# Performance work log

Hardware: AMD Instinct MI355X
Metric: run time of the kernel (lower is better)

Reference implementation:

```python
import jax, jax.numpy as jnp
import numpy as np

TOP_K = 4
N_GROUP = 8
TOPK_GROUP = 4
SCALE = 1.0

B, S, H, I, E = 2, 1024, 1024, 512, 32
SHARED_I = I * 2  # n_shared_experts = 2


def setup_inputs() -> dict:
    key = jax.random.key(0)
    ks = jax.random.split(key, 9)
    return {
        "hidden_states": jax.random.normal(ks[0], (B, S, H), jnp.float32),
        "gate_w": jax.random.normal(ks[1], (E, H), jnp.float32) * 0.02,
        "gate_bias": jnp.zeros((E,), jnp.float32),
        "gate_proj": jax.random.normal(ks[2], (E, I, H), jnp.float32) * 0.02,
        "up_proj": jax.random.normal(ks[3], (E, I, H), jnp.float32) * 0.02,
        "down_proj": jax.random.normal(ks[4], (E, H, I), jnp.float32) * 0.02,
        "shared_gate_w": jax.random.normal(ks[5], (SHARED_I, H), jnp.float32) * 0.02,
        "shared_up_w": jax.random.normal(ks[6], (SHARED_I, H), jnp.float32) * 0.02,
        "shared_down_w": jax.random.normal(ks[7], (H, SHARED_I), jnp.float32) * 0.02,
    }


def reference(hidden_states, gate_w, gate_bias, gate_proj, up_proj, down_proj,
              shared_gate_w, shared_up_w, shared_down_w):
    b, s, h = hidden_states.shape
    e = gate_w.shape[0]
    x = hidden_states.reshape(-1, h)            # (T, H)
    t = x.shape[0]

    # ---- gating (DeepSeek-V3 grouped sigmoid routing) ----
    logits = x @ gate_w.T                       # (T, E)
    scores = jax.nn.sigmoid(logits)
    sfc = scores + gate_bias[None, :]           # scores_for_choice
    # per-group score = sum of top-2 experts in group
    group_scores = jax.lax.top_k(sfc.reshape(t, N_GROUP, -1), 2)[0].sum(-1)  # (T, G)
    _, gidx = jax.lax.top_k(group_scores, TOPK_GROUP)                        # (T, topk_group)
    gmask = jax.nn.one_hot(gidx, N_GROUP, dtype=sfc.dtype).sum(1)            # (T, G)
    smask = jnp.repeat(gmask, e // N_GROUP, axis=1)                          # (T, E)
    tmp = jnp.where(smask > 0, sfc, 0.0)
    _, topk_idx = jax.lax.top_k(tmp, TOP_K)                                  # (T, K)
    topk_w = jnp.take_along_axis(scores, topk_idx, axis=1)                   # (T, K)
    topk_w = topk_w / (topk_w.sum(-1, keepdims=True) + 1e-20)                # norm_topk_prob
    topk_w = topk_w * SCALE

    # ---- routed experts (dense combine-weight formulation) ----
    comb = jnp.zeros((t, e), x.dtype).at[jnp.arange(t)[:, None], topk_idx].add(topk_w)  # (T, E)
    g = jnp.einsum('th,eih->eti', x, gate_proj)   # (E, T, I)
    u = jnp.einsum('th,eih->eti', x, up_proj)     # (E, T, I)
    a = jax.nn.silu(g) * u
    a = a * comb.T[:, :, None]                    # scale before down-proj to skip zero experts
    out = jnp.einsum('eti,ehi->th', a, down_proj) # (T, H)

    # ---- shared experts ----
    sg = x @ shared_gate_w.T
    su = x @ shared_up_w.T
    out = out + (jax.nn.silu(sg) * su) @ shared_down_w.T

    return out.reshape(b, s, h)
```

## Files before the change

kernel.cpp:

```cpp
#include <hip/hip_runtime.h>
#include <hip/hip_bf16.h>
#include <cstdint>
#include <cstddef>

#define H_DIM 1024
#define I_DIM 512
#define E_NUM 32
#define SHARED_I_DIM 1024
#define TOPK 4
#define NGROUP 8
#define TOPKG 4
#define GT 8

typedef __attribute__((ext_vector_type(8))) short bf16x8;
typedef __attribute__((ext_vector_type(4))) float f32x4;
typedef __attribute__((ext_vector_type(8))) unsigned short u16x8;

__device__ inline unsigned short f2bf(float f) {
    __hip_bfloat16 h = __float2bfloat16(f);
    return *reinterpret_cast<unsigned short*>(&h);
}
__device__ inline float bf2f(unsigned short u) {
    union { unsigned int u; float f; } w;
    w.u = ((unsigned int)u) << 16;
    return w.f;
}

__device__ inline int laddr(int row, int chunk) {
    return row * 64 + ((chunk ^ (row & 7)) << 3);
}

__global__ void init_kernel(int* cnt) {
    if (threadIdx.x < 64) cnt[threadIdx.x] = 0;
}

__global__ void cvt_kernel(const float* __restrict__ src, unsigned short* __restrict__ dst, int n8) {
    int i = blockIdx.x * blockDim.x + threadIdx.x;
    if (i >= n8) return;
    float4 a = *(const float4*)(src + (size_t)i * 8);
    float4 b = *(const float4*)(src + (size_t)i * 8 + 4);
    u16x8 v;
    v[0] = f2bf(a.x); v[1] = f2bf(a.y); v[2] = f2bf(a.z); v[3] = f2bf(a.w);
    v[4] = f2bf(b.x); v[5] = f2bf(b.y); v[6] = f2bf(b.z); v[7] = f2bf(b.w);
    *(u16x8*)(dst + (size_t)i * 8) = v;
}

__global__ __launch_bounds__(256) void gate_kernel(const float* __restrict__ x,
                                                   const float* __restrict__ gw,
                                                   float* __restrict__ logits_out) {
    int tb = blockIdx.x;
    int tid = threadIdx.x;
    __shared__ float xs[GT][H_DIM];
    __shared__ float ps[8][GT][E_NUM];
    const float* xsrc = x + (size_t)tb * GT * H_DIM;
    for (int i = tid; i < GT * H_DIM / 4; i += 256)
        ((float4*)&xs[0][0])[i] = ((const float4*)xsrc)[i];
    __syncthreads();
    int e = tid & 31, part = tid >> 5;
    const float* wrow = gw + (size_t)e * H_DIM + part * 128;
    float acc[GT] = {};
    for (int c0 = 0; c0 < 128; c0 += 32) {
        float w[32];
#pragma unroll
        for (int c = 0; c < 32; c++) w[c] = wrow[c0 + c];
#pragma unroll
        for (int t = 0; t < GT; t++) {
#pragma unroll
            for (int c = 0; c < 32; c++)
                acc[t] += w[c] * xs[t][part * 128 + c0 + c];
        }
    }
#pragma unroll
    for (int t = 0; t < GT; t++) ps[part][t][e] = acc[t];
    __syncthreads();
    {
        int t = tid >> 5, ee = tid & 31;
        float s = 0.f;
#pragma unroll
        for (int p = 0; p < 8; p++) s += ps[p][t][ee];
        logits_out[((size_t)tb * GT + t) * E_NUM + ee] = s;
    }
}

__global__ void select_kernel(const float* __restrict__ logits, const float* __restrict__ gb,
                              int* __restrict__ topk_e, float* __restrict__ topk_w,
                              int* __restrict__ cnt, int T) {
    int t = blockIdx.x * blockDim.x + threadIdx.x;
    if (t >= T) return;
    float scores[E_NUM], sfc[E_NUM];
#pragma unroll
    for (int i = 0; i < E_NUM; i++) {
        float l = logits[(size_t)t * E_NUM + i];
        float s = 1.f / (1.f + expf(-l));
        scores[i] = s;
        sfc[i] = s + gb[i];
    }
    float gs[NGROUP];
#pragma unroll
    for (int g = 0; g < NGROUP; g++) {
        float m1 = -1e30f, m2 = -1e30f;
#pragma unroll
        for (int j = 0; j < 4; j++) {
            float v = sfc[g * 4 + j];
            if (v > m1) { m2 = m1; m1 = v; }
            else if (v > m2) { m2 = v; }
        }
        gs[g] = m1 + m2;
    }
    unsigned gmask = 0;
    for (int r = 0; r < TOPKG; r++) {
        int best = 0; float bv = -1e30f;
#pragma unroll
        for (int g = 0; g < NGROUP; g++)
            if (!((gmask >> g) & 1u) && gs[g] > bv) { bv = gs[g]; best = g; }
        gmask |= 1u << best;
    }
    unsigned cmask = 0;
    int eidx[TOPK]; float ew[TOPK]; float sum = 0.f;
    for (int r = 0; r < TOPK; r++) {
        int best = 0; float bv = -1e30f; float bsc = 0.f;
#pragma unroll
        for (int i = 0; i < E_NUM; i++) {
            float v = ((gmask >> (i >> 2)) & 1u) ? sfc[i] : 0.0f;
            if (!((cmask >> i) & 1u) && v > bv) { bv = v; best = i; bsc = scores[i]; }
        }
        cmask |= 1u << best;
        eidx[r] = best; ew[r] = bsc; sum += bsc;
    }
    float inv = 1.f / (sum + 1e-20f);
#pragma unroll
    for (int k = 0; k < TOPK; k++) {
        topk_e[t * TOPK + k] = eidx[k];
        topk_w[t * TOPK + k] = ew[k] * inv;
        atomicAdd(&cnt[eidx[k]], 1);
    }
}

__global__ void scan_kernel(const int* __restrict__ cnt, int* __restrict__ off) {
    if (threadIdx.x == 0) {
        int a = 0;
        for (int e = 0; e < E_NUM; e++) { off[e] = a; a += cnt[e]; }
        off[E_NUM] = a;
    }
}

__global__ void bin_kernel(const int* __restrict__ topk_e, const float* __restrict__ topk_w,
                           const int* __restrict__ off, int* __restrict__ cnt2,
                           int* __restrict__ slot_token, float* __restrict__ slot_w,
                           int* __restrict__ slot_of, int total) {
    int i = blockIdx.x * blockDim.x + threadIdx.x;
    if (i >= total) return;
    int e = topk_e[i];
    float w = topk_w[i];
    int pos = atomicAdd(&cnt2[e], 1);
    int slot = off[e] + pos;
    slot_token[slot] = i >> 2;
    slot_w[slot] = w;
    slot_of[i] = slot;
}

__global__ __launch_bounds__(256) void combine_kernel(const unsigned short* __restrict__ out_slot,
                                                      const int* __restrict__ slot_of,
                                                      float* __restrict__ out) {
    int t = blockIdx.x;
    int h = threadIdx.x * 4;
    int s0 = slot_of[t * TOPK + 0], s1 = slot_of[t * TOPK + 1];
    int s2 = slot_of[t * TOPK + 2], s3 = slot_of[t * TOPK + 3];
    ushort4 a = *(const ushort4*)(out_slot + (size_t)s0 * H_DIM + h);
    ushort4 b = *(const ushort4*)(out_slot + (size_t)s1 * H_DIM + h);
    ushort4 c = *(const ushort4*)(out_slot + (size_t)s2 * H_DIM + h);
    ushort4 d = *(const ushort4*)(out_slot + (size_t)s3 * H_DIM + h);
    float4 o = *(float4*)(out + (size_t)t * H_DIM + h);
    o.x += bf2f(a.x) + bf2f(b.x) + bf2f(c.x) + bf2f(d.x);
    o.y += bf2f(a.y) + bf2f(b.y) + bf2f(c.y) + bf2f(d.y);
    o.z += bf2f(a.z) + bf2f(b.z) + bf2f(c.z) + bf2f(d.z);
    o.w += bf2f(a.w) + bf2f(b.w) + bf2f(c.w) + bf2f(d.w);
    *(float4*)(out + (size_t)t * H_DIM + h) = o;
}

template <int MODE, bool DUAL, int BM, bool ROUTED, bool AGATHER>
__global__ __launch_bounds__(512, 2) void gemm_kernel(
    const unsigned short* __restrict__ A, const float* __restrict__ B1,
    const float* __restrict__ B2, size_t bstride,
    void* __restrict__ Dst, int ldD,
    const int* __restrict__ slot_token, const float* __restrict__ slot_w,
    const int* __restrict__ cnt, const int* __restrict__ off_arr, int K, int Mtot) {
    static_assert(MODE != 0 || DUAL, "MODE0 requires DUAL");
    constexpr int RW = BM / 4;
    constexpr int MF = RW / 16;
    constexpr int ACH = BM / 64;
    constexpr int TPR = 512 / BM;

    int itile, mtile, e;
    if constexpr (ROUTED) { e = blockIdx.x; itile = blockIdx.y; mtile = blockIdx.z; }
    else                  { itile = blockIdx.x; mtile = blockIdx.y; e = 0; }
    int count = Mtot, base = 0;
    if (ROUTED) {
        count = cnt[e];
        base = off_arr[e];
        if (mtile * BM >= count) return;
    }

    __shared__ __align__(16) unsigned short As[2][BM * 64];
    __shared__ __align__(16) unsigned short Bs1[2][64 * 64];
    __shared__ __align__(16) unsigned short Bs2[2][DUAL ? 64 * 64 : 8];

    int tid = threadIdx.x;

    int as_row = tid / TPR;
    int as_cb = (tid % TPR) * ACH;
    int am = mtile * BM + as_row;
    int ar;
    if (AGATHER)      ar = (am < count) ? slot_token[base + am] : 0;
    else if (ROUTED)  ar = base + ((am < count) ? am : 0);
    else              ar = (am < count) ? am : 0;
    const unsigned short* Arow = A + (size_t)ar * K + as_cb * 8;

    int bs_row = tid >> 3, bs_ch = tid & 7;
    const float* B1r = B1 + (size_t)e * bstride + (size_t)(itile * 64 + bs_row) * K + bs_ch * 8;
    const float* B2r = DUAL ? (B2 + (size_t)e * bstride + (size_t)(itile * 64 + bs_row) * K + bs_ch * 8)
                            : nullptr;

    f32x4 acc1[MF][2] = {};
    f32x4 acc2[DUAL ? MF : 1][2] = {};

    int lane = tid & 63, wid = tid >> 6;
    int wrow = (wid >> 1) * RW, wcol = (wid & 1) * 32;
    int frow = lane & 15, fch = lane >> 4;

    u16x8 pA0[ACH], pA1[ACH];
    float4 b1lo0, b1hi0, b1lo1, b1hi1;
    float4 b2lo0, b2hi0, b2lo1, b2hi1;

    auto loadS = [&](u16x8* pA, float4& b1lo, float4& b1hi, float4& b2lo, float4& b2hi, int k0) {
#pragma unroll
        for (int c = 0; c < ACH; c++) pA[c] = *(const u16x8*)(Arow + k0 + c * 8);
        b1lo = *(const float4*)(B1r + k0);
        b1hi = *(const float4*)(B1r + k0 + 4);
        if constexpr (DUAL) {
            b2lo = *(const float4*)(B2r + k0);
            b2hi = *(const float4*)(B2r + k0 + 4);
        }
    };
    auto writeS = [&](int buf, const u16x8* pA, float4 b1lo, float4 b1hi, float4 b2lo, float4 b2hi) {
        unsigned short* As_ = As[buf];
        unsigned short* Bs1_ = Bs1[buf];
#pragma unroll
        for (int c = 0; c < ACH; c++)
            *(u16x8*)(&As_[laddr(as_row, as_cb + c)]) = pA[c];
        u16x8 s;
        s[0] = f2bf(b1lo.x); s[1] = f2bf(b1lo.y); s[2] = f2bf(b1lo.z); s[3] = f2bf(b1lo.w);
        s[4] = f2bf(b1hi.x); s[5] = f2bf(b1hi.y); s[6] = f2bf(b1hi.z); s[7] = f2bf(b1hi.w);
        *(u16x8*)(&Bs1_[laddr(bs_row, bs_ch)]) = s;
        if constexpr (DUAL) {
            unsigned short* Bs2_ = Bs2[buf];
            u16x8 s2;
            s2[0] = f2bf(b2lo.x); s2[1] = f2bf(b2lo.y); s2[2] = f2bf(b2lo.z); s2[3] = f2bf(b2lo.w);
            s2[4] = f2bf(b2hi.x); s2[5] = f2bf(b2hi.y); s2[6] = f2bf(b2hi.z); s2[7] = f2bf(b2hi.w);
            *(u16x8*)(&Bs2_[laddr(bs_row, bs_ch)]) = s2;
        }
    };
    auto compute = [&](int buf) {
        const unsigned short* As_ = As[buf];
        const unsigned short* Bs1_ = Bs1[buf];
        const unsigned short* Bs2_ = Bs2[buf];
#pragma unroll
        for (int kk = 0; kk < 2; kk++) {
            int cb = fch + kk * 4;
            bf16x8 bf1[2], bf2[DUAL ? 2 : 1], af[MF];
#pragma unroll
            for (int nf = 0; nf < 2; nf++)
                bf1[nf] = *(const bf16x8*)(&Bs1_[laddr(wcol + nf * 16 + frow, cb)]);
            if constexpr (DUAL) {
#pragma unroll
                for (int nf = 0; nf < 2; nf++)
                    bf2[nf] = *(const bf16x8*)(&Bs2_[laddr(wcol + nf * 16 + frow, cb)]);
            }
#pragma unroll
            for (int mf = 0; mf < MF; mf++)
                af[mf] = *(const bf16x8*)(&As_[laddr(wrow + mf * 16 + frow, cb)]);
#pragma unroll
            for (int mf = 0; mf < MF; mf++)
#pragma unroll
                for (int nf = 0; nf < 2; nf++) {
                    acc1[mf][nf] = __builtin_amdgcn_mfma_f32_16x16x32_bf16(af[mf], bf1[nf], acc1[mf][nf], 0, 0, 0);
                    if constexpr (DUAL)
                        acc2[mf][nf] = __builtin_amdgcn_mfma_f32_16x16x32_bf16(af[mf], bf2[nf], acc2[mf][nf], 0, 0, 0);
                }
        }
    };

    const int NK = K >> 6;
    loadS(pA0, b1lo0, b1hi0, b2lo0, b2hi0, 0);
    loadS(pA1, b1lo1, b1hi1, b2lo1, b2hi1, 64);
    writeS(0, pA0, b1lo0, b1hi0, b2lo0, b2hi0);
    loadS(pA0, b1lo0, b1hi0, b2lo0, b2hi0, 128);
    __syncthreads();
    for (int it = 0; it < NK; it += 2) {
        writeS(1, pA1, b1lo1, b1hi1, b2lo1, b2hi1);
        if (it + 3 < NK) loadS(pA1, b1lo1, b1hi1, b2lo1, b2hi1, (it + 3) << 6);
        compute(0);
        __syncthreads();
        if (it + 2 < NK) {
            writeS(0, pA0, b1lo0, b1hi0, b2lo0, b2hi0);
            if (it + 4 < NK) loadS(pA0, b1lo0, b1hi0, b2lo0, b2hi0, (it + 4) << 6);
        }
        compute(1);
        if (it + 2 < NK) __syncthreads();
    }

#pragma unroll
    for (int mf = 0; mf < MF; mf++)
#pragma unroll
        for (int nf = 0; nf < 2; nf++)
#pragma unroll
            for (int j = 0; j < 4; j++) {
                int rloc = wrow + mf * 16 + (lane >> 4) * 4 + j;
                int mrow = mtile * BM + rloc;
                int col = itile * 64 + wcol + nf * 16 + (lane & 15);
                if (mrow >= count) continue;
                if constexpr (MODE == 0) {
                    float w = ROUTED ? slot_w[base + mrow] : 1.0f;
                    float g = acc1[mf][nf][j];
                    float a = (g / (1.f + __expf(-g))) * acc2[mf][nf][j] * w;
                    ((unsigned short*)Dst)[(size_t)(base + mrow) * ldD + col] = f2bf(a);
                } else if constexpr (MODE == 1) {
                    ((float*)Dst)[(size_t)mrow * ldD + col] = acc1[mf][nf][j];
                } else {
                    ((unsigned short*)Dst)[(size_t)(base + mrow) * ldD + col] = f2bf(acc1[mf][nf][j]);
                }
            }
}

extern "C" void kernel_launch(void* const* d_in, const int* in_sizes, int n_in,
                              void* d_out, int out_size, void* d_ws, size_t ws_size,
                              hipStream_t stream) {
    const float* x = (const float*)d_in[0];
    const float* gw = (const float*)d_in[1];
    const float* gb = (const float*)d_in[2];
    const float* gate_proj = (const float*)d_in[3];
    const float* up_proj = (const float*)d_in[4];
    const float* down_proj = (const float*)d_in[5];
    const float* sgw = (const float*)d_in[6];
    const float* suw = (const float*)d_in[7];
    const float* sdw = (const float*)d_in[8];
    float* out = (float*)d_out;

    const int T = in_sizes[0] / H_DIM;
    const int total_slots = T * TOPK;

    char* ws = (char*)d_ws;
    int* cnt = (int*)ws;
    int* cnt2 = cnt + 32;
    int* off = cnt + 64;
    int* topk_e = cnt + 128;
    float* topk_w = (float*)(topk_e + total_slots);
    int* slot_token = (int*)(topk_w + total_slots);
    float* slot_w = (float*)(slot_token + total_slots);
    int* slot_of = (int*)(slot_w + total_slots);
    float* logits = (float*)(slot_of + total_slots);
    unsigned short* x_bf = (unsigned short*)(logits + (size_t)T * E_NUM);
    unsigned short* act_r = x_bf + (size_t)T * H_DIM;
    unsigned short* act_s = act_r + (size_t)(total_slots + 256) * I_DIM;
    unsigned short* out_slot = act_s + (size_t)T * SHARED_I_DIM;

    hipLaunchKernelGGL(init_kernel, dim3(1), dim3(64), 0, stream, cnt);
    hipLaunchKernelGGL(cvt_kernel, dim3((T * H_DIM / 8 + 255) / 256), dim3(256), 0, stream,
                       x, x_bf, T * H_DIM / 8);
    hipLaunchKernelGGL(gate_kernel, dim3(T / GT), dim3(256), 0, stream, x, gw, logits);
    hipLaunchKernelGGL(select_kernel, dim3((T + 255) / 256), dim3(256), 0, stream,
                       logits, gb, topk_e, topk_w, cnt, T);
    hipLaunchKernelGGL(scan_kernel, dim3(1), dim3(1), 0, stream, cnt, off);
    hipLaunchKernelGGL(bin_kernel, dim3((total_slots + 255) / 256), dim3(256), 0, stream,
                       topk_e, topk_w, off, cnt2, slot_token, slot_w, slot_of, total_slots);

    hipLaunchKernelGGL((gemm_kernel<0, true, 256, true, true>),
                       dim3(E_NUM, I_DIM / 64, 32), dim3(512), 0, stream,
                       x_bf, gate_proj, up_proj, (size_t)I_DIM * H_DIM,
                       (void*)act_r, I_DIM, slot_token, slot_w, cnt, off, H_DIM, 0);

    hipLaunchKernelGGL((gemm_kernel<0, true, 128, false, false>),
                       dim3(SHARED_I_DIM / 64, T / 128, 1), dim3(512), 0, stream,
                       x_bf, sgw, suw, (size_t)0,
                       (void*)act_s, SHARED_I_DIM, (const int*)nullptr, (const float*)nullptr,
                       (const int*)nullptr, (const int*)nullptr, H_DIM, T);

    hipLaunchKernelGGL((gemm_kernel<1, false, 128, false, false>),
                       dim3(H_DIM / 64, T / 128, 1), dim3(512), 0, stream,
                       act_s, sdw, (const float*)nullptr, (size_t)0,
                       (void*)out, H_DIM, (const int*)nullptr, (const float*)nullptr,
                       (const int*)nullptr, (const int*)nullptr, SHARED_I_DIM, T);

    hipLaunchKernelGGL((gemm_kernel<3, false, 256, true, false>),
                       dim3(E_NUM, H_DIM / 64, 32), dim3(512), 0, stream,
                       act_r, down_proj, (const float*)nullptr, (size_t)H_DIM * I_DIM,
                       (void*)out_slot, H_DIM, slot_token, (const float*)nullptr, cnt, off, I_DIM, 0);

    hipLaunchKernelGGL(combine_kernel, dim3(T), dim3(256), 0, stream, out_slot, slot_of, out);
}
```

Measured before the change: 204.5 us.

## Shrink GEMM tiles to 64x64 with K-step 32 and 256-thread blocks

```diff
diff --git a/kernel.cpp b/kernel.cpp
--- a/kernel.cpp
+++ b/kernel.cpp
@@ -27,7 +27,7 @@
 }
 
 __device__ inline int laddr(int row, int chunk) {
-    return row * 64 + ((chunk ^ (row & 7)) << 3);
+    return row * 32 + ((chunk ^ ((row >> 1) & 3)) << 3);
 }
 
 __global__ void init_kernel(int* cnt) {
@@ -178,18 +178,14 @@
     *(float4*)(out + (size_t)t * H_DIM + h) = o;
 }
 
-template <int MODE, bool DUAL, int BM, bool ROUTED, bool AGATHER>
-__global__ __launch_bounds__(512, 2) void gemm_kernel(
+template <int MODE, bool DUAL, bool ROUTED, bool AGATHER>
+__global__ __launch_bounds__(256, 2) void gemm_kernel(
     const unsigned short* __restrict__ A, const float* __restrict__ B1,
     const float* __restrict__ B2, size_t bstride,
     void* __restrict__ Dst, int ldD,
     const int* __restrict__ slot_token, const float* __restrict__ slot_w,
     const int* __restrict__ cnt, const int* __restrict__ off_arr, int K, int Mtot) {
     static_assert(MODE != 0 || DUAL, "MODE0 requires DUAL");
-    constexpr int RW = BM / 4;
-    constexpr int MF = RW / 16;
-    constexpr int ACH = BM / 64;
-    constexpr int TPR = 512 / BM;
 
     int itile, mtile, e;
     if constexpr (ROUTED) { e = blockIdx.x; itile = blockIdx.y; mtile = blockIdx.z; }
@@ -198,43 +194,40 @@
     if (ROUTED) {
         count = cnt[e];
         base = off_arr[e];
-        if (mtile * BM >= count) return;
-    }
-
-    __shared__ __align__(16) unsigned short As[2][BM * 64];
-    __shared__ __align__(16) unsigned short Bs1[2][64 * 64];
-    __shared__ __align__(16) unsigned short Bs2[2][DUAL ? 64 * 64 : 8];
+        if (mtile * 64 >= count) return;
+    }
+
+    __shared__ __align__(16) unsigned short As[2][64 * 32];
+    __shared__ __align__(16) unsigned short Bs1[2][64 * 32];
+    __shared__ __align__(16) unsigned short Bs2[2][DUAL ? 64 * 32 : 8];
 
     int tid = threadIdx.x;
-
-    int as_row = tid / TPR;
-    int as_cb = (tid % TPR) * ACH;
-    int am = mtile * BM + as_row;
+    int srow = tid >> 2, sch = tid & 3;
+
+    int am = mtile * 64 + srow;
     int ar;
     if (AGATHER)      ar = (am < count) ? slot_token[base + am] : 0;
     else if (ROUTED)  ar = base + ((am < count) ? am : 0);
     else              ar = (am < count) ? am : 0;
-    const unsigned short* Arow = A + (size_t)ar * K + as_cb * 8;
-
-    int bs_row = tid >> 3, bs_ch = tid & 7;
-    const float* B1r = B1 + (size_t)e * bstride + (size_t)(itile * 64 + bs_row) * K + bs_ch * 8;
-    const float* B2r = DUAL ? (B2 + (size_t)e * bstride + (size_t)(itile * 64 + bs_row) * K + bs_ch * 8)
-                            : nullptr;
-
-    f32x4 acc1[MF][2] = {};
-    f32x4 acc2[DUAL ? MF : 1][2] = {};
+    const unsigned short* Arow = A + (size_t)ar * K + sch * 8;
+
+    int bn = itile * 64 + srow;
+    const float* B1r = B1 + (size_t)e * bstride + (size_t)bn * K + sch * 8;
+    const float* B2r = DUAL ? (B2 + (size_t)e * bstride + (size_t)bn * K + sch * 8) : nullptr;
+
+    f32x4 acc1[2][2] = {};
+    f32x4 acc2[DUAL ? 2 : 1][2] = {};
 
     int lane = tid & 63, wid = tid >> 6;
-    int wrow = (wid >> 1) * RW, wcol = (wid & 1) * 32;
+    int wrow = (wid >> 1) * 32, wcol = (wid & 1) * 32;
     int frow = lane & 15, fch = lane >> 4;
 
-    u16x8 pA0[ACH], pA1[ACH];
+    u16x8 pA0, pA1;
     float4 b1lo0, b1hi0, b1lo1, b1hi1;
     float4 b2lo0, b2hi0, b2lo1, b2hi1;
 
-    auto loadS = [&](u16x8* pA, float4& b1lo, float4& b1hi, float4& b2lo, float4& b2hi, int k0) {
-#pragma unroll
-        for (int c = 0; c < ACH; c++) pA[c] = *(const u16x8*)(Arow + k0 + c * 8);
+    auto loadS = [&](u16x8& pA, float4& b1lo, float4& b1hi, float4& b2lo, float4& b2hi, int k0) {
+        pA = *(const u16x8*)(Arow + k0);
         b1lo = *(const float4*)(B1r + k0);
         b1hi = *(const float4*)(B1r + k0 + 4);
         if constexpr (DUAL) {
@@ -242,81 +235,75 @@
             b2hi = *(const float4*)(B2r + k0 + 4);
         }
     };
-    auto writeS = [&](int buf, const u16x8* pA, float4 b1lo, float4 b1hi, float4 b2lo, float4 b2hi) {
-        unsigned short* As_ = As[buf];
-        unsigned short* Bs1_ = Bs1[buf];
-#pragma unroll
-        for (int c = 0; c < ACH; c++)
-            *(u16x8*)(&As_[laddr(as_row, as_cb + c)]) = pA[c];
+    auto writeS = [&](int buf, u16x8 pA, float4 b1lo, float4 b1hi, float4 b2lo, float4 b2hi) {
+        *(u16x8*)(&As[buf][laddr(srow, sch)]) = pA;
         u16x8 s;
         s[0] = f2bf(b1lo.x); s[1] = f2bf(b1lo.y); s[2] = f2bf(b1lo.z); s[3] = f2bf(b1lo.w);
         s[4] = f2bf(b1hi.x); s[5] = f2bf(b1hi.y); s[6] = f2bf(b1hi.z); s[7] = f2bf(b1hi.w);
-        *(u16x8*)(&Bs1_[laddr(bs_row, bs_ch)]) = s;
+        *(u16x8*)(&Bs1[buf][laddr(srow, sch)]) = s;
         if constexpr (DUAL) {
-            unsigned short* Bs2_ = Bs2[buf];
             u16x8 s2;
             s2[0] = f2bf(b2lo.x); s2[1] = f2bf(b2lo.y); s2[2] = f2bf(b2lo.z); s2[3] = f2bf(b2lo.w);
             s2[4] = f2bf(b2hi.x); s2[5] = f2bf(b2hi.y); s2[6] = f2bf(b2hi.z); s2[7] = f2bf(b2hi.w);
-            *(u16x8*)(&Bs2_[laddr(bs_row, bs_ch)]) = s2;
+            *(u16x8*)(&Bs2[buf][laddr(srow, sch)]) = s2;
         }
     };
     auto compute = [&](int buf) {
-        const unsigned short* As_ = As[buf];
-        const unsigned short* Bs1_ = Bs1[buf];
-        const unsigned short* Bs2_ = Bs2[buf];
-#pragma unroll
-        for (int kk = 0; kk < 2; kk++) {
-            int cb = fch + kk * 4;
-            bf16x8 bf1[2], bf2[DUAL ? 2 : 1], af[MF];
-#pragma unroll
-            for (int nf = 0; nf < 2; nf++)
-                bf1[nf] = *(const bf16x8*)(&Bs1_[laddr(wcol + nf * 16 + frow, cb)]);
-            if constexpr (DUAL) {
-#pragma unroll
-                for (int nf = 0; nf < 2; nf++)
-                    bf2[nf] = *(const bf16x8*)(&Bs2_[laddr(wcol + nf * 16 + frow, cb)]);
+        bf16x8 af[2], b1[2], b2[DUAL ? 2 : 1];
+#pragma unroll
+        for (int nf = 0; nf < 2; nf++) {
+            int r = wcol + nf * 16 + frow;
+            b1[nf] = *(const bf16x8*)(&Bs1[buf][laddr(r, fch)]);
+        }
+        if constexpr (DUAL) {
+#pragma unroll
+            for (int nf = 0; nf < 2; nf++) {
+                int r = wcol + nf * 16 + frow;
+                b2[nf] = *(const bf16x8*)(&Bs2[buf][laddr(r, fch)]);
             }
-#pragma unroll
-            for (int mf = 0; mf < MF; mf++)
-                af[mf] = *(const bf16x8*)(&As_[laddr(wrow + mf * 16 + frow, cb)]);
-#pragma unroll
-            for (int mf = 0; mf < MF; mf++)
-#pragma unroll
-                for (int nf = 0; nf < 2; nf++) {
-                    acc1[mf][nf] = __builtin_amdgcn_mfma_f32_16x16x32_bf16(af[mf], bf1[nf], acc1[mf][nf], 0, 0, 0);
-                    if constexpr (DUAL)
-                        acc2[mf][nf] = __builtin_amdgcn_mfma_f32_16x16x32_bf16(af[mf], bf2[nf], acc2[mf][nf], 0, 0, 0);
-                }
-        }
+        }
+#pragma unroll
+        for (int mf = 0; mf < 2; mf++) {
+            int r = wrow + mf * 16 + frow;
+            af[mf] = *(const bf16x8*)(&As[buf][laddr(r, fch)]);
+        }
+#pragma unroll
+        for (int mf = 0; mf < 2; mf++)
+#pragma unroll
+            for (int nf = 0; nf < 2; nf++) {
+                acc1[mf][nf] = __builtin_amdgcn_mfma_f32_16x16x32_bf16(af[mf], b1[nf], acc1[mf][nf], 0, 0, 0);
+                if constexpr (DUAL)
+                    acc2[mf][nf] = __builtin_amdgcn_mfma_f32_16x16x32_bf16(af[mf], b2[nf], acc2[mf][nf], 0, 0, 0);
+            }
     };
 
-    const int NK = K >> 6;
+    const int NK = K >> 5;
     loadS(pA0, b1lo0, b1hi0, b2lo0, b2hi0, 0);
-    loadS(pA1, b1lo1, b1hi1, b2lo1, b2hi1, 64);
+    loadS(pA1, b1lo1, b1hi1, b2lo1, b2hi1, 32);
     writeS(0, pA0, b1lo0, b1hi0, b2lo0, b2hi0);
-    loadS(pA0, b1lo0, b1hi0, b2lo0, b2hi0, 128);
+    loadS(pA0, b1lo0, b1hi0, b2lo0, b2hi0, 64);
     __syncthreads();
     for (int it = 0; it < NK; it += 2) {
         writeS(1, pA1, b1lo1, b1hi1, b2lo1, b2hi1);
-        if (it + 3 < NK) loadS(pA1, b1lo1, b1hi1, b2lo1, b2hi1, (it + 3) << 6);
+        if (it + 3 < NK) loadS(pA1, b1lo1, b1hi1, b2lo1, b2hi1, (it + 3) << 5);
         compute(0);
         __syncthreads();
         if (it + 2 < NK) {
             writeS(0, pA0, b1lo0, b1hi0, b2lo0, b2hi0);
-            if (it + 4 < NK) loadS(pA0, b1lo0, b1hi0, b2lo0, b2hi0, (it + 4) << 6);
+            if (it + 4 < NK) loadS(pA0, b1lo0, b1hi0, b2lo0, b2hi0, (it + 4) << 5);
         }
         compute(1);
         if (it + 2 < NK) __syncthreads();
     }
 
 #pragma unroll
-    for (int mf = 0; mf < MF; mf++)
+    for (int mf = 0; mf < 2; mf++)
 #pragma unroll
         for (int nf = 0; nf < 2; nf++)
 #pragma unroll
             for (int j = 0; j < 4; j++) {
                 int rloc = wrow + mf * 16 + (lane >> 4) * 4 + j;
-                int mrow = mtile * BM + rloc;
+                int mrow = mtile * 64 + rloc;
                 int col = itile * 64 + wcol + nf * 16 + (lane & 15);
                 if (mrow >= count) continue;
                 if constexpr (MODE == 0) {
@@ -361,7 +348,7 @@
     float* logits = (float*)(slot_of + total_slots);
     unsigned short* x_bf = (unsigned short*)(logits + (size_t)T * E_NUM);
     unsigned short* act_r = x_bf + (size_t)T * H_DIM;
-    unsigned short* act_s = act_r + (size_t)(total_slots + 256) * I_DIM;
+    unsigned short* act_s = act_r + (size_t)(total_slots + 64) * I_DIM;
     unsigned short* out_slot = act_s + (size_t)T * SHARED_I_DIM;
 
     hipLaunchKernelGGL(init_kernel, dim3(1), dim3(64), 0, stream, cnt);
@@ -374,25 +361,25 @@
     hipLaunchKernelGGL(bin_kernel, dim3((total_slots + 255) / 256), dim3(256), 0, stream,
                        topk_e, topk_w, off, cnt2, slot_token, slot_w, slot_of, total_slots);
 
-    hipLaunchKernelGGL((gemm_kernel<0, true, 256, true, true>),
-                       dim3(E_NUM, I_DIM / 64, 32), dim3(512), 0, stream,
+    hipLaunchKernelGGL((gemm_kernel<0, true, true, true>),
+                       dim3(E_NUM, I_DIM / 64, 32), dim3(256), 0, stream,
                        x_bf, gate_proj, up_proj, (size_t)I_DIM * H_DIM,
                        (void*)act_r, I_DIM, slot_token, slot_w, cnt, off, H_DIM, 0);
 
-    hipLaunchKernelGGL((gemm_kernel<0, true, 128, false, false>),
-                       dim3(SHARED_I_DIM / 64, T / 128, 1), dim3(512), 0, stream,
+    hipLaunchKernelGGL((gemm_kernel<0, true, false, false>),
+                       dim3(SHARED_I_DIM / 64, T / 64, 1), dim3(256), 0, stream,
                        x_bf, sgw, suw, (size_t)0,
                        (void*)act_s, SHARED_I_DIM, (const int*)nullptr, (const float*)nullptr,
                        (const int*)nullptr, (const int*)nullptr, H_DIM, T);
 
-    hipLaunchKernelGGL((gemm_kernel<1, false, 128, false, false>),
-                       dim3(H_DIM / 64, T / 128, 1), dim3(512), 0, stream,
+    hipLaunchKernelGGL((gemm_kernel<1, false, false, false>),
+                       dim3(H_DIM / 64, T / 64, 1), dim3(256), 0, stream,
                        act_s, sdw, (const float*)nullptr, (size_t)0,
                        (void*)out, H_DIM, (const int*)nullptr, (const float*)nullptr,
                        (const int*)nullptr, (const int*)nullptr, SHARED_I_DIM, T);
 
-    hipLaunchKernelGGL((gemm_kernel<3, false, 256, true, false>),
-                       dim3(E_NUM, H_DIM / 64, 32), dim3(512), 0, stream,
+    hipLaunchKernelGGL((gemm_kernel<3, false, true, false>),
+                       dim3(E_NUM, H_DIM / 64, 32), dim3(256), 0, stream,
                        act_r, down_proj, (const float*)nullptr, (size_t)H_DIM * I_DIM,
                        (void*)out_slot, H_DIM, slot_token, (const float*)nullptr, cnt, off, I_DIM, 0);
 
```

Result: slower. 225.9 us (+10.5%).
